# Kernel optimization log

Hardware: AMD Instinct MI355X
Metric: run time of the kernel (lower is better)

Reference implementation:

```python
import jax, jax.numpy as jnp
import numpy as np

SAMPLE_RATE = 44100.0


def _peaking_coeffs(freq, gain_db, q, fs):
    """RBJ cookbook peaking-EQ biquad coefficients (as in dasp-pytorch).
    freq/gain_db/q: [B, K]. Returns normalized b0,b1,b2,a1,a2 each [B, K]."""
    A = jnp.power(10.0, gain_db / 40.0)
    w0 = 2.0 * jnp.pi * freq / fs
    cosw = jnp.cos(w0)
    alpha = jnp.sin(w0) / (2.0 * q)
    b0 = 1.0 + alpha * A
    b1 = -2.0 * cosw
    b2 = 1.0 - alpha * A
    a0 = 1.0 + alpha / A
    a1 = -2.0 * cosw
    a2 = 1.0 - alpha / A
    inv_a0 = 1.0 / a0
    return b0 * inv_a0, b1 * inv_a0, b2 * inv_a0, a1 * inv_a0, a2 * inv_a0


def setup_inputs() -> dict:
    key = jax.random.key(0)
    k1, k2, k3, k4 = jax.random.split(key, 4)
    B, C, T, K = 32, 2, 262144, 6
    audio = jax.random.normal(k1, (B, C, T), dtype=jnp.float32) * 0.1
    # realistic EQ parameter ranges
    frequencies = 100.0 + jax.random.uniform(k2, (B, K), dtype=jnp.float32) * 9900.0  # 100 Hz .. 10 kHz
    gains = jax.random.normal(k3, (B, K), dtype=jnp.float32) * 6.0                     # ~ +/- 6 dB
    q_factors = 0.5 + jax.random.uniform(k4, (B, K), dtype=jnp.float32) * 3.0          # 0.5 .. 3.5
    return {"audio": audio, "frequencies": frequencies, "gains": gains, "q_factors": q_factors}


def reference(audio, frequencies, gains, q_factors):
    # audio: [B, C, T]; per-batch cascade of K peaking biquads over time.
    B, C, T = audio.shape
    K = frequencies.shape[1]
    b0, b1, b2, a1, a2 = _peaking_coeffs(frequencies, gains, q_factors, SAMPLE_RATE)
    # [K, B, 1] for broadcasting over channels
    b0, b1, b2, a1, a2 = (jnp.transpose(c)[:, :, None] for c in (b0, b1, b2, a1, a2))

    def step(carry, x):  # x: [B, C], one time sample through the whole cascade
        s1, s2 = carry  # each [K, B, C], direct-form II transposed states
        y = x
        ns1, ns2 = [], []
        for k in range(K):  # small fixed band loop (structurally sequential cascade)
            yk = b0[k] * y + s1[k]
            ns1.append(b1[k] * y - a1[k] * yk + s2[k])
            ns2.append(b2[k] * y - a2[k] * yk)
            y = yk
        return (jnp.stack(ns1), jnp.stack(ns2)), y

    init = (jnp.zeros((K, B, C), audio.dtype), jnp.zeros((K, B, C), audio.dtype))
    xs = jnp.moveaxis(audio, 2, 0)  # [T, B, C]
    _, ys = jax.lax.scan(step, init, xs)
    return jnp.moveaxis(ys, 0, 2)  # [B, C, T]
```

## Files before the change

kernel.cpp:

```cpp
#include <hip/hip_runtime.h>
#include <math.h>

namespace {
constexpr int B = 32, C = 2, T = 262144, K = 6;
constexpr int SEG = 2048;
constexpr int L = T / SEG;
constexpr int NBC = B * C;
constexpr int NST = 2 * K;
constexpr int LOG2L = 7;
constexpr int TS = 16;
constexpr int NT = L / TS;
constexpr int WPB = SEG / 64;
constexpr int GP = 8;
constexpr int NW = 4;
constexpr float FS = 44100.0f;
}

__device__ __forceinline__ float rl(float v, int lane) {
  return __int_as_float(__builtin_amdgcn_readlane(__float_as_int(v), lane));
}

__device__ __forceinline__ void ld12(const float* p, float (&v)[NST]) {
  const float4* q = reinterpret_cast<const float4*>(p);
  float4 a = q[0], b4 = q[1], c4 = q[2];
  v[0] = a.x; v[1] = a.y; v[2] = a.z; v[3] = a.w;
  v[4] = b4.x; v[5] = b4.y; v[6] = b4.z; v[7] = b4.w;
  v[8] = c4.x; v[9] = c4.y; v[10] = c4.z; v[11] = c4.w;
}

__device__ __forceinline__ void st12(float* p, const float (&v)[NST]) {
  float4* q = reinterpret_cast<float4*>(p);
  q[0] = make_float4(v[0], v[1], v[2], v[3]);
  q[1] = make_float4(v[4], v[5], v[6], v[7]);
  q[2] = make_float4(v[8], v[9], v[10], v[11]);
}

__device__ __forceinline__ void affine(const float (&M)[NST][NST], float (&s)[NST],
                                       const float (&z)[NST]) {
  float ns[NST];
#pragma unroll
  for (int r = 0; r < NST; ++r) {
    float a = z[r];
#pragma unroll
    for (int m = 0; m < NST; ++m) a = fmaf(M[r][m], s[m], a);
    ns[r] = a;
  }
#pragma unroll
  for (int r = 0; r < NST; ++r) s[r] = ns[r];
}

__global__ void eq_coeffs(const float* __restrict__ fr, const float* __restrict__ gn,
                          const float* __restrict__ qf, float* __restrict__ cf) {
  int i = blockIdx.x * blockDim.x + threadIdx.x;
  if (i >= B * K) return;
  float f = fr[i], g = gn[i], Q = qf[i];
  float A  = powf(10.0f, g * (1.0f / 40.0f));
  float w0 = 6.283185307179586f * f / FS;
  float cw = cosf(w0);
  float al = sinf(w0) / (2.0f * Q);
  float b0 = 1.0f + al * A;
  float b1 = -2.0f * cw;
  float b2 = 1.0f - al * A;
  float a0 = 1.0f + al / A;
  float a2 = 1.0f - al / A;
  float ia = 1.0f / a0;
  float* p = cf + i * 5;
  p[0] = b0 * ia; p[1] = b1 * ia; p[2] = b2 * ia; p[3] = b1 * ia; p[4] = a2 * ia;
}

template <bool WRITE_OUT>
__global__ __launch_bounds__(64, 2) void eq_pass(const float* __restrict__ x,
                                                 const float* __restrict__ cf,
                                                 const float* __restrict__ st_in,
                                                 float* __restrict__ st_out,
                                                 float* __restrict__ y) {
  __shared__ float sIn[2][64][17];
  __shared__ float sOut[2][64][17];

  int l = threadIdx.x;
  int wid = blockIdx.x;
  int bc = wid / WPB;
  int segbase = (wid % WPB) * 64;
  int b = bc / C;
  int tid = bc * SEG + segbase + l;

  const float4* xp4 = reinterpret_cast<const float4*>(x + (size_t)bc * T + (size_t)segbase * L);
  float4* yp4 = reinterpret_cast<float4*>(y + (size_t)bc * T + (size_t)segbase * L);
  constexpr int Q4 = L / 4;

  int sj = l >> 2;
  int qj = l & 3;

  float4 ra[4], rb[4];
#pragma unroll
  for (int j = 0; j < 4; ++j) ra[j] = xp4[(size_t)(j * 16 + sj) * Q4 + qj];
#pragma unroll
  for (int j = 0; j < 4; ++j) rb[j] = xp4[(size_t)(j * 16 + sj) * Q4 + 4 + qj];

  float b0[K], b1c[K], b2c[K], a1c[K], a2c[K];
#pragma unroll
  for (int k = 0; k < K; ++k) {
    const float* p = cf + (b * K + k) * 5;
    b0[k] = p[0]; b1c[k] = p[1]; b2c[k] = p[2]; a1c[k] = p[3]; a2c[k] = p[4];
  }

  float s1[K], s2[K];
  if (WRITE_OUT) {
    float st[NST];
    ld12(st_in + (size_t)tid * NST, st);
#pragma unroll
    for (int k = 0; k < K; ++k) { s1[k] = st[2 * k]; s2[k] = st[2 * k + 1]; }
  } else {
#pragma unroll
    for (int k = 0; k < K; ++k) { s1[k] = 0.0f; s2[k] = 0.0f; }
  }

  auto tile = [&](float4 (&r)[4], int t, int pb) {
#pragma unroll
    for (int j = 0; j < 4; ++j) {
      int seg = j * 16 + sj;
      sIn[pb][seg][qj * 4 + 0] = r[j].x;
      sIn[pb][seg][qj * 4 + 1] = r[j].y;
      sIn[pb][seg][qj * 4 + 2] = r[j].z;
      sIn[pb][seg][qj * 4 + 3] = r[j].w;
    }
    if (t + 2 < NT) {
#pragma unroll
      for (int j = 0; j < 4; ++j)
        r[j] = xp4[(size_t)(j * 16 + sj) * Q4 + (size_t)(t + 2) * 4 + qj];
    }
    float out16[TS];
#pragma unroll
    for (int i = 0; i < TS; ++i) {
      float yv = sIn[pb][l][i];
#pragma unroll
      for (int k = 0; k < K; ++k) {
        float yk = fmaf(b0[k], yv, s1[k]);
        float t1 = fmaf(b1c[k], yv, s2[k]);
        s1[k] = fmaf(-a1c[k], yk, t1);
        float t2 = b2c[k] * yv;
        s2[k] = fmaf(-a2c[k], yk, t2);
        yv = yk;
      }
      out16[i] = yv;
    }
    if (WRITE_OUT) {
#pragma unroll
      for (int i = 0; i < TS; ++i) sOut[pb][l][i] = out16[i];
#pragma unroll
      for (int j = 0; j < 4; ++j) {
        int seg = j * 16 + sj;
        float4 o;
        o.x = sOut[pb][seg][qj * 4 + 0];
        o.y = sOut[pb][seg][qj * 4 + 1];
        o.z = sOut[pb][seg][qj * 4 + 2];
        o.w = sOut[pb][seg][qj * 4 + 3];
        yp4[(size_t)seg * Q4 + (size_t)t * 4 + qj] = o;
      }
    }
  };

  for (int tt = 0; tt < NT; tt += 2) {
    tile(ra, tt, 0);
    tile(rb, tt + 1, 1);
  }

  if (!WRITE_OUT) {
    float st[NST];
#pragma unroll
    for (int k = 0; k < K; ++k) { st[2 * k] = s1[k]; st[2 * k + 1] = s2[k]; }
    st12(st_out + (size_t)tid * NST, st);
  }
}

__global__ __launch_bounds__(256, 1) void eq_scan(const float* __restrict__ cf,
                                                  const float* __restrict__ zsf,
                                                  float* __restrict__ sif) {
  __shared__ float PhiL[NST][NST];
  __shared__ float Rg[NST][NST + 1];
  __shared__ float Rw[NST][NST + 1];
  __shared__ float FB[NW][64][NST + 1];
  __shared__ float SL[NW][64][NST + 1];
  __shared__ float WF[NW][NST + 1];

  int bc = blockIdx.x;
  int b = bc / C;
  int t = threadIdx.x;
  int w = t >> 6;
  int l = t & 63;
  bool act = (l < NST);

  float b0[K], b1c[K], b2c[K], a1c[K], a2c[K];
#pragma unroll
  for (int k = 0; k < K; ++k) {
    const float* p = cf + (b * K + k) * 5;
    b0[k] = p[0]; b1c[k] = p[1]; b2c[k] = p[2]; a1c[k] = p[3]; a2c[k] = p[4];
  }

  float col[NST];
  {
    float s1[K], s2[K];
#pragma unroll
    for (int k = 0; k < K; ++k) {
      s1[k] = (l == 2 * k) ? 1.0f : 0.0f;
      s2[k] = (l == 2 * k + 1) ? 1.0f : 0.0f;
    }
    float yv = 0.0f;
#pragma unroll
    for (int k = 0; k < K; ++k) {
      float yk = fmaf(b0[k], yv, s1[k]);
      float t1 = fmaf(b1c[k], yv, s2[k]);
      float ns1 = fmaf(-a1c[k], yk, t1);
      float ns2 = fmaf(-a2c[k], yk, b2c[k] * yv);
      s1[k] = ns1; s2[k] = ns2; yv = yk;
    }
#pragma unroll
    for (int k = 0; k < K; ++k) { col[2 * k] = s1[k]; col[2 * k + 1] = s2[k]; }
  }

  auto square = [&]() {
    float nc[NST];
#pragma unroll
    for (int r = 0; r < NST; ++r) nc[r] = 0.0f;
#pragma unroll
    for (int m = 0; m < NST; ++m) {
      float wv = col[m];
#pragma unroll
      for (int r = 0; r < NST; ++r) nc[r] = fmaf(rl(col[r], m), wv, nc[r]);
    }
#pragma unroll
    for (int r = 0; r < NST; ++r) col[r] = nc[r];
  };

  for (int p = 0; p < LOG2L; ++p) square();
  if (w == 0 && act) {
#pragma unroll
    for (int r = 0; r < NST; ++r) PhiL[r][l] = col[r];
  }
  for (int p = 0; p < 3; ++p) square();
  if (w == 0 && act) {
#pragma unroll
    for (int r = 0; r < NST; ++r) Rg[r][l] = col[r];
  }
  for (int p = 0; p < 6; ++p) square();
  if (w == 0 && act) {
#pragma unroll
    for (int r = 0; r < NST; ++r) Rw[r][l] = col[r];
  }
  __syncthreads();

  float rowg[NST], roww[NST];
#pragma unroll
  for (int m = 0; m < NST; ++m) {
    rowg[m] = act ? Rg[l][m] : 0.0f;
    roww[m] = act ? Rw[l][m] : 0.0f;
  }
  float phi[NST][NST];
#pragma unroll
  for (int r = 0; r < NST; ++r)
#pragma unroll
    for (int m = 0; m < NST; ++m) phi[r][m] = PhiL[r][m];

  const float* zb = zsf + ((size_t)bc * SEG + (size_t)t * GP) * NST;
  float s[NST];
  ld12(zb, s);
#pragma unroll
  for (int j = 1; j < GP; ++j) {
    float zc[NST];
    ld12(zb + (size_t)j * NST, zc);
    affine(phi, s, zc);
  }
#pragma unroll
  for (int r = 0; r < NST; ++r) FB[w][l][r] = s[r];
  __syncthreads();

  {
    float sv = 0.0f;
    for (int i = 0; i < 64; ++i) {
      float wv = act ? FB[w][i][l] : 0.0f;
      float t0 = fmaf(rowg[0], rl(sv, 0), fmaf(rowg[1], rl(sv, 1), rowg[2] * rl(sv, 2)));
      float t1 = fmaf(rowg[3], rl(sv, 3), fmaf(rowg[4], rl(sv, 4), rowg[5] * rl(sv, 5)));
      float t2 = fmaf(rowg[6], rl(sv, 6), fmaf(rowg[7], rl(sv, 7), rowg[8] * rl(sv, 8)));
      float t3 = fmaf(rowg[9], rl(sv, 9), fmaf(rowg[10], rl(sv, 10), rowg[11] * rl(sv, 11)));
      sv = ((t0 + t1) + (t2 + t3)) + wv;
    }
    if (act) WF[w][l] = sv;
  }
  __syncthreads();

  float swv = 0.0f;
  for (int w2 = 0; w2 < w; ++w2) {
    float wfv = act ? WF[w2][l] : 0.0f;
    float t0 = fmaf(roww[0], rl(swv, 0), fmaf(roww[1], rl(swv, 1), roww[2] * rl(swv, 2)));
    float t1 = fmaf(roww[3], rl(swv, 3), fmaf(roww[4], rl(swv, 4), roww[5] * rl(swv, 5)));
    float t2 = fmaf(roww[6], rl(swv, 6), fmaf(roww[7], rl(swv, 7), roww[8] * rl(swv, 8)));
    float t3 = fmaf(roww[9], rl(swv, 9), fmaf(roww[10], rl(swv, 10), roww[11] * rl(swv, 11)));
    swv = ((t0 + t1) + (t2 + t3)) + wfv;
  }

  {
    float sv = swv;
    for (int i = 0; i < 64; ++i) {
      if (act) SL[w][i][l] = sv;
      float wv = act ? FB[w][i][l] : 0.0f;
      float t0 = fmaf(rowg[0], rl(sv, 0), fmaf(rowg[1], rl(sv, 1), rowg[2] * rl(sv, 2)));
      float t1 = fmaf(rowg[3], rl(sv, 3), fmaf(rowg[4], rl(sv, 4), rowg[5] * rl(sv, 5)));
      float t2 = fmaf(rowg[6], rl(sv, 6), fmaf(rowg[7], rl(sv, 7), rowg[8] * rl(sv, 8)));
      float t3 = fmaf(rowg[9], rl(sv, 9), fmaf(rowg[10], rl(sv, 10), rowg[11] * rl(sv, 11)));
      sv = ((t0 + t1) + (t2 + t3)) + wv;
    }
  }
  __syncthreads();

  float sg[NST];
#pragma unroll
  for (int r = 0; r < NST; ++r) sg[r] = SL[w][l][r];
  float* ob = sif + ((size_t)bc * SEG + (size_t)t * GP) * NST;
#pragma unroll
  for (int j = 0; j < GP; ++j) {
    st12(ob + (size_t)j * NST, sg);
    if (j + 1 < GP) {
      float zc[NST];
      ld12(zb + (size_t)j * NST, zc);
      affine(phi, sg, zc);
    }
  }
}

extern "C" void kernel_launch(void* const* d_in, const int* in_sizes, int n_in,
                              void* d_out, int out_size, void* d_ws, size_t ws_size,
                              hipStream_t stream) {
  const float* audio = (const float*)d_in[0];
  const float* fr    = (const float*)d_in[1];
  const float* gn    = (const float*)d_in[2];
  const float* qf    = (const float*)d_in[3];
  float* out = (float*)d_out;

  float* cf  = (float*)d_ws;
  float* zsf = cf + B * K * 5;
  float* sif = zsf + (size_t)NBC * SEG * NST;

  hipLaunchKernelGGL(eq_coeffs, dim3((B * K + 63) / 64), dim3(64), 0, stream,
                     fr, gn, qf, cf);
  hipLaunchKernelGGL((eq_pass<false>), dim3(NBC * WPB), dim3(64), 0, stream,
                     audio, cf, nullptr, zsf, out);
  hipLaunchKernelGGL(eq_scan, dim3(NBC), dim3(256), 0, stream, cf, zsf, sif);
  hipLaunchKernelGGL((eq_pass<true>), dim3(NBC * WPB), dim3(64), 0, stream,
                     audio, cf, sif, nullptr, out);
}
```

Before: 87.26 us.

## Process two segments per thread to interleave independent biquad recurrences

Each thread of eq_pass now filters two independent segments (128 rows per 64-thread block), interleaving their biquad cascade FMAs so two dependency chains run at once and hide FMA latency. The double-buffered tile lambda is replaced by a single LDS buffer with one-tile-ahead prefetch of eight float4 loads, and launch bounds drop to one block per SIMD. The trade-off is half as many blocks (fewer waves in flight) and more registers per thread; the single shared buffer may also need extra synchronization care, since the 64-thread block is a single wave.

Measured after the change: 91.59 us. +5.0%, slower.

```diff
diff --git a/kernel.cpp b/kernel.cpp
--- a/kernel.cpp
+++ b/kernel.cpp
@@ -8,9 +8,12 @@
 constexpr int NBC = B * C;
 constexpr int NST = 2 * K;
 constexpr int LOG2L = 7;
+constexpr int RPB = 128;
+constexpr int WPB = SEG / RPB;
 constexpr int TS = 16;
 constexpr int NT = L / TS;
-constexpr int WPB = SEG / 64;
+constexpr int Q4 = L / 4;
+constexpr int PIN = 17;
 constexpr int GP = 8;
 constexpr int NW = 4;
 constexpr float FS = 44100.0f;
@@ -69,33 +72,31 @@
 }
 
 template <bool WRITE_OUT>
-__global__ __launch_bounds__(64, 2) void eq_pass(const float* __restrict__ x,
+__global__ __launch_bounds__(64, 1) void eq_pass(const float* __restrict__ x,
                                                  const float* __restrict__ cf,
                                                  const float* __restrict__ st_in,
                                                  float* __restrict__ st_out,
                                                  float* __restrict__ y) {
-  __shared__ float sIn[2][64][17];
-  __shared__ float sOut[2][64][17];
+  __shared__ float sIn[RPB][PIN];
+  __shared__ float sOut[WRITE_OUT ? RPB : 1][WRITE_OUT ? PIN : 1];
 
   int l = threadIdx.x;
   int wid = blockIdx.x;
   int bc = wid / WPB;
-  int segbase = (wid % WPB) * 64;
+  int segbase = (wid % WPB) * RPB;
   int b = bc / C;
-  int tid = bc * SEG + segbase + l;
+  int tidA = bc * SEG + segbase + l;
+  int tidB = tidA + 64;
 
   const float4* xp4 = reinterpret_cast<const float4*>(x + (size_t)bc * T + (size_t)segbase * L);
   float4* yp4 = reinterpret_cast<float4*>(y + (size_t)bc * T + (size_t)segbase * L);
-  constexpr int Q4 = L / 4;
 
   int sj = l >> 2;
   int qj = l & 3;
 
-  float4 ra[4], rb[4];
-#pragma unroll
-  for (int j = 0; j < 4; ++j) ra[j] = xp4[(size_t)(j * 16 + sj) * Q4 + qj];
-#pragma unroll
-  for (int j = 0; j < 4; ++j) rb[j] = xp4[(size_t)(j * 16 + sj) * Q4 + 4 + qj];
+  float4 r[8];
+#pragma unroll
+  for (int j = 0; j < 8; ++j) r[j] = xp4[(size_t)(j * 16 + sj) * Q4 + qj];
 
   float b0[K], b1c[K], b2c[K], a1c[K], a2c[K];
 #pragma unroll
@@ -104,72 +105,78 @@
     b0[k] = p[0]; b1c[k] = p[1]; b2c[k] = p[2]; a1c[k] = p[3]; a2c[k] = p[4];
   }
 
-  float s1[K], s2[K];
+  float s1a[K], s2a[K], s1b[K], s2b[K];
   if (WRITE_OUT) {
     float st[NST];
-    ld12(st_in + (size_t)tid * NST, st);
-#pragma unroll
-    for (int k = 0; k < K; ++k) { s1[k] = st[2 * k]; s2[k] = st[2 * k + 1]; }
+    ld12(st_in + (size_t)tidA * NST, st);
+#pragma unroll
+    for (int k = 0; k < K; ++k) { s1a[k] = st[2 * k]; s2a[k] = st[2 * k + 1]; }
+    ld12(st_in + (size_t)tidB * NST, st);
+#pragma unroll
+    for (int k = 0; k < K; ++k) { s1b[k] = st[2 * k]; s2b[k] = st[2 * k + 1]; }
   } else {
 #pragma unroll
-    for (int k = 0; k < K; ++k) { s1[k] = 0.0f; s2[k] = 0.0f; }
-  }
-
-  auto tile = [&](float4 (&r)[4], int t, int pb) {
-#pragma unroll
-    for (int j = 0; j < 4; ++j) {
-      int seg = j * 16 + sj;
-      sIn[pb][seg][qj * 4 + 0] = r[j].x;
-      sIn[pb][seg][qj * 4 + 1] = r[j].y;
-      sIn[pb][seg][qj * 4 + 2] = r[j].z;
-      sIn[pb][seg][qj * 4 + 3] = r[j].w;
-    }
-    if (t + 2 < NT) {
-#pragma unroll
-      for (int j = 0; j < 4; ++j)
-        r[j] = xp4[(size_t)(j * 16 + sj) * Q4 + (size_t)(t + 2) * 4 + qj];
-    }
-    float out16[TS];
+    for (int k = 0; k < K; ++k) { s1a[k] = 0.0f; s2a[k] = 0.0f; s1b[k] = 0.0f; s2b[k] = 0.0f; }
+  }
+
+  for (int t = 0; t < NT; ++t) {
+#pragma unroll
+    for (int j = 0; j < 8; ++j) {
+      int row = j * 16 + sj;
+      sIn[row][qj * 4 + 0] = r[j].x;
+      sIn[row][qj * 4 + 1] = r[j].y;
+      sIn[row][qj * 4 + 2] = r[j].z;
+      sIn[row][qj * 4 + 3] = r[j].w;
+    }
+    if (t + 1 < NT) {
+#pragma unroll
+      for (int j = 0; j < 8; ++j)
+        r[j] = xp4[(size_t)(j * 16 + sj) * Q4 + (size_t)(t + 1) * 4 + qj];
+    }
+    float xa[TS], xb[TS];
+#pragma unroll
+    for (int i = 0; i < TS; ++i) { xa[i] = sIn[l][i]; xb[i] = sIn[64 + l][i]; }
 #pragma unroll
     for (int i = 0; i < TS; ++i) {
-      float yv = sIn[pb][l][i];
+      float ya = xa[i], yb = xb[i];
 #pragma unroll
       for (int k = 0; k < K; ++k) {
-        float yk = fmaf(b0[k], yv, s1[k]);
-        float t1 = fmaf(b1c[k], yv, s2[k]);
-        s1[k] = fmaf(-a1c[k], yk, t1);
-        float t2 = b2c[k] * yv;
-        s2[k] = fmaf(-a2c[k], yk, t2);
-        yv = yk;
+        float yka = fmaf(b0[k], ya, s1a[k]);
+        float ykb = fmaf(b0[k], yb, s1b[k]);
+        float t1a = fmaf(b1c[k], ya, s2a[k]);
+        float t1b = fmaf(b1c[k], yb, s2b[k]);
+        s1a[k] = fmaf(-a1c[k], yka, t1a);
+        s1b[k] = fmaf(-a1c[k], ykb, t1b);
+        float t2a = b2c[k] * ya;
+        float t2b = b2c[k] * yb;
+        s2a[k] = fmaf(-a2c[k], yka, t2a);
+        s2b[k] = fmaf(-a2c[k], ykb, t2b);
+        ya = yka; yb = ykb;
       }
-      out16[i] = yv;
+      if (WRITE_OUT) { sOut[l][i] = ya; sOut[64 + l][i] = yb; }
     }
     if (WRITE_OUT) {
 #pragma unroll
-      for (int i = 0; i < TS; ++i) sOut[pb][l][i] = out16[i];
-#pragma unroll
-      for (int j = 0; j < 4; ++j) {
-        int seg = j * 16 + sj;
+      for (int j = 0; j < 8; ++j) {
+        int row = j * 16 + sj;
         float4 o;
-        o.x = sOut[pb][seg][qj * 4 + 0];
-        o.y = sOut[pb][seg][qj * 4 + 1];
-        o.z = sOut[pb][seg][qj * 4 + 2];
-        o.w = sOut[pb][seg][qj * 4 + 3];
-        yp4[(size_t)seg * Q4 + (size_t)t * 4 + qj] = o;
+        o.x = sOut[row][qj * 4 + 0];
+        o.y = sOut[row][qj * 4 + 1];
+        o.z = sOut[row][qj * 4 + 2];
+        o.w = sOut[row][qj * 4 + 3];
+        yp4[(size_t)row * Q4 + (size_t)t * 4 + qj] = o;
       }
     }
-  };
-
-  for (int tt = 0; tt < NT; tt += 2) {
-    tile(ra, tt, 0);
-    tile(rb, tt + 1, 1);
   }
 
   if (!WRITE_OUT) {
     float st[NST];
 #pragma unroll
-    for (int k = 0; k < K; ++k) { st[2 * k] = s1[k]; st[2 * k + 1] = s2[k]; }
-    st12(st_out + (size_t)tid * NST, st);
+    for (int k = 0; k < K; ++k) { st[2 * k] = s1a[k]; st[2 * k + 1] = s2a[k]; }
+    st12(st_out + (size_t)tidA * NST, st);
+#pragma unroll
+    for (int k = 0; k < K; ++k) { st[2 * k] = s1b[k]; st[2 * k + 1] = s2b[k]; }
+    st12(st_out + (size_t)tidB * NST, st);
   }
 }
 
```
